# Kernel tuning notes

Measured on AMD Instinct MI355X. Metric: run time of the kernel, lower is better.

## Reference

```python
import jax, jax.numpy as jnp
import numpy as np

B, T, C = 1024, 512, 48

def setup_inputs() -> dict:
    key = jax.random.key(0)
    k1, k2, k3 = jax.random.split(key, 3)
    potentials = jax.random.normal(k1, (B, T, C), dtype=jnp.float32)
    sequence_lengths = jax.random.randint(k2, (B, 1), 1, T).astype(jnp.int32)
    # layer weight: uniform initializer (keras default uniform is U[-0.05, 0.05])
    transitions = jax.random.uniform(k3, (C, C), dtype=jnp.float32, minval=-0.05, maxval=0.05)
    return {"potentials": potentials, "sequence_lengths": sequence_lengths, "transitions": transitions}

def reference(potentials, sequence_lengths, transitions):
    # Faithful jax port of tf.contrib.crf.crf_decode (Viterbi max-plus DP),
    # followed by one_hot as in CRFLayer.call (inference branch of in_train_phase).
    Bb, Tt, Cc = potentials.shape
    seq_len = sequence_lengths.reshape(-1)  # K.flatten

    def fwd_step(score, xs):
        # score: [B,C] viterbi scores at step t-1
        pot_t, t = xs
        total = score[:, :, None] + transitions[None]  # [B, C_prev, C_cur]
        bp = jnp.argmax(total, axis=1).astype(jnp.int32)  # [B,C] best prev tag
        new_score = jnp.max(total, axis=1) + pot_t        # [B,C]
        valid = (t < seq_len)[:, None]                    # mask steps past seq_len
        score = jnp.where(valid, new_score, score)
        bp = jnp.where(valid, bp, jnp.arange(Cc, dtype=jnp.int32)[None])
        return score, bp

    init = potentials[:, 0]                               # [B,C]
    xs = (jnp.swapaxes(potentials[:, 1:], 0, 1), jnp.arange(1, Tt))
    last_score, bps = jax.lax.scan(fwd_step, init, xs)    # bps: [T-1,B,C]

    last_tag = jnp.argmax(last_score, axis=-1).astype(jnp.int32)  # [B]

    def back_step(tag_next, bp):
        prev = jnp.take_along_axis(bp, tag_next[:, None], axis=1)[:, 0]
        return prev, tag_next

    first_tag, tags_rest = jax.lax.scan(back_step, last_tag, bps, reverse=True)
    tags = jnp.concatenate([first_tag[None], tags_rest], axis=0)  # [T,B]
    tags = jnp.swapaxes(tags, 0, 1)                               # [B,T]
    return jax.nn.one_hot(tags, Cc, dtype=potentials.dtype)       # [B,T,C]
```

## Files before the change

kernel.cpp:

```cpp
#include <hip/hip_runtime.h>

#define T_DIM 512
#define C_DIM 48
#define BPS   64
#define CH    4

typedef float f32x2 __attribute__((ext_vector_type(2)));
typedef float f32x4 __attribute__((ext_vector_type(4)));

#if __has_builtin(__builtin_amdgcn_readlane)
#define READLANE_I(v, l) __builtin_amdgcn_readlane((v), (l))
#else
#define READLANE_I(v, l) __shfl((v), (l), 64)
#endif

#if __has_builtin(__builtin_amdgcn_wave_barrier)
#define WAVE_SYNC() do { __asm__ __volatile__("" ::: "memory"); __builtin_amdgcn_wave_barrier(); } while (0)
#else
#define WAVE_SYNC() __asm__ __volatile__("" ::: "memory")
#endif

__device__ __forceinline__ unsigned umin_(unsigned a, unsigned b) { return a < b ? a : b; }

__device__ __forceinline__ float max3f(float a, float b, float c) {
    float d;
    asm("v_max3_f32 %0, %1, %2, %3" : "=v"(d) : "v"(a), "v"(b), "v"(c));
    return d;
}
__device__ __forceinline__ unsigned min3u(unsigned a, unsigned b, unsigned c) {
    unsigned d;
    asm("v_min3_u32 %0, %1, %2, %3" : "=v"(d) : "v"(a), "v"(b), "v"(c));
    return d;
}

#define CV(I_)  (cv2[(I_) / 2][(I_) & 1])
#define UU(I_)  (__float_as_uint(d2[(I_) / 2][(I_) & 1]) | (unsigned)(I_))
#define EMIN3(I_) min3u(UU(I_), UU((I_) + 1), UU((I_) + 2))

#define VSTEP(T_, PV_) do {                                                  \
    float A0  = max3f(CV(0),  CV(1),  CV(2));                                \
    float A1  = max3f(CV(3),  CV(4),  CV(5));                                \
    float A2  = max3f(CV(6),  CV(7),  CV(8));                                \
    float A3  = max3f(CV(9),  CV(10), CV(11));                               \
    float A4  = max3f(CV(12), CV(13), CV(14));                               \
    float A5  = max3f(CV(15), CV(16), CV(17));                               \
    float A6  = max3f(CV(18), CV(19), CV(20));                               \
    float A7  = max3f(CV(21), CV(22), CV(23));                               \
    float A8  = max3f(CV(24), CV(25), CV(26));                               \
    float A9  = max3f(CV(27), CV(28), CV(29));                               \
    float A10 = max3f(CV(30), CV(31), CV(32));                               \
    float A11 = max3f(CV(33), CV(34), CV(35));                               \
    float A12 = max3f(CV(36), CV(37), CV(38));                               \
    float A13 = max3f(CV(39), CV(40), CV(41));                               \
    float A14 = max3f(CV(42), CV(43), CV(44));                               \
    float A15 = max3f(CV(45), CV(46), CV(47));                               \
    float B0 = max3f(A0,  A1,  A2);                                          \
    float B1 = max3f(A3,  A4,  A5);                                          \
    float B2 = max3f(A6,  A7,  A8);                                          \
    float B3 = max3f(A9,  A10, A11);                                         \
    float B4 = max3f(A12, A13, A14);                                         \
    float Cx0 = max3f(B0, B1, B2);                                           \
    float Cx1 = max3f(B3, B4, A15);                                          \
    const float m_v = fmaxf(Cx0, Cx1);                                       \
    const float ns_ = m_v + (PV_);                                           \
    const int nxt_ = cur ^ 1;                                                \
    sc[nxt_][tid] = ns_;                            \
    WAVE_SYNC();                                                             \
    const f32x4* sp_ = (const f32x4*)sc[nxt_];                               \
    f32x4 sv_[12];                                                           \
    _Pragma("unroll")                                                        \
    for (int m_ = 0; m_ < 12; ++m_) sv_[m_] = sp_[m_];      \
           \
    f32x2 d2[24];                                                            \
    const f32x2 mv2_ = {m_v, m_v};                                           \
    _Pragma("unroll")                                                        \
    for (int k_ = 0; k_ < 24; ++k_) d2[k_] = cv2[k_] - mv2_;     \
    unsigned U0  = EMIN3(0);   unsigned U1  = EMIN3(3);                      \
    unsigned U2  = EMIN3(6);   unsigned U3  = EMIN3(9);                      \
    unsigned U4  = EMIN3(12);  unsigned U5  = EMIN3(15);                     \
    unsigned U6  = EMIN3(18);  unsigned U7  = EMIN3(21);                     \
    unsigned U8  = EMIN3(24);  unsigned U9  = EMIN3(27);                     \
    unsigned U10 = EMIN3(30);  unsigned U11 = EMIN3(33);                     \
    unsigned U12 = EMIN3(36);  unsigned U13 = EMIN3(39);                     \
    unsigned U14 = EMIN3(42);  unsigned U15 = EMIN3(45);                     \
    unsigned V0 = min3u(U0,  U1,  U2);                                       \
    unsigned V1 = min3u(U3,  U4,  U5);                                       \
    unsigned V2 = min3u(U6,  U7,  U8);                                       \
    unsigned V3 = min3u(U9,  U10, U11);                                      \
    unsigned V4 = min3u(U12, U13, U14);                                      \
    unsigned W0 = min3u(V0, V1, V2);                                         \
    unsigned W1 = min3u(V3, V4, U15);                                        \
    const unsigned wi_ = umin_(W0, W1);                                      \
    bp[(T_) * BPS + tid] = (unsigned char)wi_;     \
         \
    _Pragma("unroll")                                                        \
    for (int m_ = 0; m_ < 12; ++m_) {                                        \
        cv2[2 * m_]     = sv_[m_].xy + tc2[2 * m_];                          \
        cv2[2 * m_ + 1] = sv_[m_].zw + tc2[2 * m_ + 1];                      \
    }                                                                        \
    cur = nxt_;                                                              \
} while (0)

__global__ __launch_bounds__(64, 1) void crf_viterbi(
    const float* __restrict__ pot,
    const int*   __restrict__ seqlen,
    const float* __restrict__ trans,
    float*       __restrict__ out)
{
    const int b   = blockIdx.x;
    const int tid = threadIdx.x;
    const int jj  = (tid < C_DIM) ? tid : (C_DIM - 1);

    __shared__ __align__(16) float sc[2][64];
    __shared__ unsigned char bp[T_DIM * BPS];
    __shared__ __align__(4) unsigned char tags[T_DIM];

    const float* potb = pot + (size_t)b * (T_DIM * C_DIM);
    const int L   = seqlen[b];
    const int thi = L - 1;

    f32x2 tc2[24];
#pragma unroll
    for (int k = 0; k < 24; ++k) {
        tc2[k][0] = trans[(2 * k)     * C_DIM + jj];
        tc2[k][1] = trans[(2 * k + 1) * C_DIM + jj];
    }

    sc[0][tid] = potb[jj];
    WAVE_SYNC();
    f32x2 cv2[24];
    {
        const f32x4* sp0 = (const f32x4*)sc[0];
#pragma unroll
        for (int m = 0; m < 12; ++m) {
            f32x4 sv = sp0[m];
            cv2[2 * m]     = sv.xy + tc2[2 * m];
            cv2[2 * m + 1] = sv.zw + tc2[2 * m + 1];
        }
    }
    int cur = 0;

    const float* pp = potb + jj;

    float pb[CH];
#pragma unroll
    for (int k = 0; k < CH; ++k) {
        int tt = 1 + k; if (tt > T_DIM - 1) tt = T_DIM - 1;
        pb[k] = pp[tt * C_DIM];
    }
    for (int t0 = 1; t0 < L; t0 += CH) {
        float nb[CH];
#pragma unroll
        for (int k = 0; k < CH; ++k) {
            int tt = t0 + CH + k; if (tt > T_DIM - 1) tt = T_DIM - 1;
            nb[k] = pp[tt * C_DIM];
        }
#pragma unroll
        for (int k = 0; k < CH; ++k) {
            const int t = t0 + k;
            if (t >= L) break;
            VSTEP(t, pb[k]);
        }
#pragma unroll
        for (int k = 0; k < CH; ++k) pb[k] = nb[k];
    }
    __syncthreads();

    const float* fs = sc[cur];
    float bv = fs[0];
    int   bi = 0;
#pragma unroll
    for (int i = 1; i < C_DIM; ++i) {
        float v = fs[i];
        if (v > bv) { bv = v; bi = i; }
    }
    const int last_tag = __builtin_amdgcn_readfirstlane(bi);

    for (int t = L + tid; t < T_DIM; t += 64) tags[t] = (unsigned char)last_tag;

    int y = last_tag;
    for (int c0 = (thi >> 6) << 6; c0 >= 0; c0 -= 64) {
        int row[64];
#pragma unroll
        for (int k = 0; k < 64; ++k) row[k] = bp[(c0 + k) * BPS + jj];

        int vacc = 0;
#pragma unroll
        for (int k = 63; k >= 0; --k) {
            const int t = c0 + k;
            vacc = (tid == k) ? y : vacc;
            const int ynew = READLANE_I(row[k], y);
            if ((unsigned)(t - 1) < (unsigned)thi) y = ynew;
        }
        const int tk = c0 + tid;
        if (tk <= thi) tags[tk] = (unsigned char)(vacc & 0xff);
    }
    __syncthreads();

    if (tid < C_DIM) {
        const int r = tid / 12;
        const int q = tid - r * 12;
        const int cbase = q * 4;
        float* ob = out + (size_t)b * (T_DIM * C_DIM);
        for (int t0 = 0; t0 < T_DIM; t0 += 4) {
            const unsigned int tg4 = *(const unsigned int*)&tags[t0];
            const int mytag = (int)((tg4 >> (r * 8)) & 0xffu);
            float4 v;
            v.x = (cbase + 0 == mytag) ? 1.0f : 0.0f;
            v.y = (cbase + 1 == mytag) ? 1.0f : 0.0f;
            v.z = (cbase + 2 == mytag) ? 1.0f : 0.0f;
            v.w = (cbase + 3 == mytag) ? 1.0f : 0.0f;
            *(float4*)(ob + (size_t)(t0 + r) * C_DIM + cbase) = v;
        }
    }
}

extern "C" void kernel_launch(void* const* d_in, const int* in_sizes, int n_in,
                              void* d_out, int out_size, void* d_ws, size_t ws_size,
                              hipStream_t stream) {
    const float* pot    = (const float*)d_in[0];
    const int*   sl     = (const int*)d_in[1];
    const float* trans  = (const float*)d_in[2];
    float*       out    = (float*)d_out;
    const int B = in_sizes[1];
    crf_viterbi<<<B, 64, 0, stream>>>(pot, sl, trans, out);
}
```

Baseline: 345.0 us.

## Split Viterbi forward into max-wave and argmax-wave producer/consumer pipeline

The forward recursion now runs on two waves per block. Wave 0 does only the max-plus score update and writes scores and maxima into shared-memory ring buffers. Wave 1 rebuilds the candidate values from the ring and computes the argmax backpointers, which takes the argmax off wave 0's serial critical path. The waves coordinate through volatile shared progress counters with spin-waits. The one-hot output store is also spread over 96 threads instead of 48. The cost is spin-wait overhead, recomputing the candidate values on wave 1, and doubled register pressure per block under launch_bounds(128,2).

```diff
diff --git a/kernel.cpp b/kernel.cpp
--- a/kernel.cpp
+++ b/kernel.cpp
@@ -4,6 +4,8 @@
 #define C_DIM 48
 #define BPS   64
 #define CH    4
+#define RING  8
+#define RMASK (RING - 1)
 
 typedef float f32x2 __attribute__((ext_vector_type(2)));
 typedef float f32x4 __attribute__((ext_vector_type(4)));
@@ -14,6 +16,12 @@
 #define READLANE_I(v, l) __shfl((v), (l), 64)
 #endif
 
+#if __has_builtin(__builtin_amdgcn_s_sleep)
+#define SPIN_PAUSE() __builtin_amdgcn_s_sleep(1)
+#else
+#define SPIN_PAUSE()
+#endif
+
 #if __has_builtin(__builtin_amdgcn_wave_barrier)
 #define WAVE_SYNC() do { __asm__ __volatile__("" ::: "memory"); __builtin_amdgcn_wave_barrier(); } while (0)
 #else
@@ -37,83 +45,25 @@
 #define UU(I_)  (__float_as_uint(d2[(I_) / 2][(I_) & 1]) | (unsigned)(I_))
 #define EMIN3(I_) min3u(UU(I_), UU((I_) + 1), UU((I_) + 2))
 
-#define VSTEP(T_, PV_) do {                                                  \
-    float A0  = max3f(CV(0),  CV(1),  CV(2));                                \
-    float A1  = max3f(CV(3),  CV(4),  CV(5));                                \
-    float A2  = max3f(CV(6),  CV(7),  CV(8));                                \
-    float A3  = max3f(CV(9),  CV(10), CV(11));                               \
-    float A4  = max3f(CV(12), CV(13), CV(14));                               \
-    float A5  = max3f(CV(15), CV(16), CV(17));                               \
-    float A6  = max3f(CV(18), CV(19), CV(20));                               \
-    float A7  = max3f(CV(21), CV(22), CV(23));                               \
-    float A8  = max3f(CV(24), CV(25), CV(26));                               \
-    float A9  = max3f(CV(27), CV(28), CV(29));                               \
-    float A10 = max3f(CV(30), CV(31), CV(32));                               \
-    float A11 = max3f(CV(33), CV(34), CV(35));                               \
-    float A12 = max3f(CV(36), CV(37), CV(38));                               \
-    float A13 = max3f(CV(39), CV(40), CV(41));                               \
-    float A14 = max3f(CV(42), CV(43), CV(44));                               \
-    float A15 = max3f(CV(45), CV(46), CV(47));                               \
-    float B0 = max3f(A0,  A1,  A2);                                          \
-    float B1 = max3f(A3,  A4,  A5);                                          \
-    float B2 = max3f(A6,  A7,  A8);                                          \
-    float B3 = max3f(A9,  A10, A11);                                         \
-    float B4 = max3f(A12, A13, A14);                                         \
-    float Cx0 = max3f(B0, B1, B2);                                           \
-    float Cx1 = max3f(B3, B4, A15);                                          \
-    const float m_v = fmaxf(Cx0, Cx1);                                       \
-    const float ns_ = m_v + (PV_);                                           \
-    const int nxt_ = cur ^ 1;                                                \
-    sc[nxt_][tid] = ns_;                            \
-    WAVE_SYNC();                                                             \
-    const f32x4* sp_ = (const f32x4*)sc[nxt_];                               \
-    f32x4 sv_[12];                                                           \
-    _Pragma("unroll")                                                        \
-    for (int m_ = 0; m_ < 12; ++m_) sv_[m_] = sp_[m_];      \
-           \
-    f32x2 d2[24];                                                            \
-    const f32x2 mv2_ = {m_v, m_v};                                           \
-    _Pragma("unroll")                                                        \
-    for (int k_ = 0; k_ < 24; ++k_) d2[k_] = cv2[k_] - mv2_;     \
-    unsigned U0  = EMIN3(0);   unsigned U1  = EMIN3(3);                      \
-    unsigned U2  = EMIN3(6);   unsigned U3  = EMIN3(9);                      \
-    unsigned U4  = EMIN3(12);  unsigned U5  = EMIN3(15);                     \
-    unsigned U6  = EMIN3(18);  unsigned U7  = EMIN3(21);                     \
-    unsigned U8  = EMIN3(24);  unsigned U9  = EMIN3(27);                     \
-    unsigned U10 = EMIN3(30);  unsigned U11 = EMIN3(33);                     \
-    unsigned U12 = EMIN3(36);  unsigned U13 = EMIN3(39);                     \
-    unsigned U14 = EMIN3(42);  unsigned U15 = EMIN3(45);                     \
-    unsigned V0 = min3u(U0,  U1,  U2);                                       \
-    unsigned V1 = min3u(U3,  U4,  U5);                                       \
-    unsigned V2 = min3u(U6,  U7,  U8);                                       \
-    unsigned V3 = min3u(U9,  U10, U11);                                      \
-    unsigned V4 = min3u(U12, U13, U14);                                      \
-    unsigned W0 = min3u(V0, V1, V2);                                         \
-    unsigned W1 = min3u(V3, V4, U15);                                        \
-    const unsigned wi_ = umin_(W0, W1);                                      \
-    bp[(T_) * BPS + tid] = (unsigned char)wi_;     \
-         \
-    _Pragma("unroll")                                                        \
-    for (int m_ = 0; m_ < 12; ++m_) {                                        \
-        cv2[2 * m_]     = sv_[m_].xy + tc2[2 * m_];                          \
-        cv2[2 * m_ + 1] = sv_[m_].zw + tc2[2 * m_ + 1];                      \
-    }                                                                        \
-    cur = nxt_;                                                              \
-} while (0)
-
-__global__ __launch_bounds__(64, 1) void crf_viterbi(
+__global__ __launch_bounds__(128, 2) void crf_viterbi(
     const float* __restrict__ pot,
     const int*   __restrict__ seqlen,
     const float* __restrict__ trans,
     float*       __restrict__ out)
 {
-    const int b   = blockIdx.x;
-    const int tid = threadIdx.x;
-    const int jj  = (tid < C_DIM) ? tid : (C_DIM - 1);
-
-    __shared__ __align__(16) float sc[2][64];
+    const int b    = blockIdx.x;
+    const int tid  = threadIdx.x;
+    const int lane = tid & 63;
+    const int wid  = tid >> 6;
+    const int jj   = (lane < C_DIM) ? lane : (C_DIM - 1);
+
+    __shared__ __align__(16) float sring[RING][64];
+    __shared__ __align__(16) float mring[RING][64];
     __shared__ unsigned char bp[T_DIM * BPS];
     __shared__ __align__(4) unsigned char tags[T_DIM];
+    __shared__ __align__(16) float fsc[64];
+    __shared__ volatile int prog0;
+    __shared__ volatile int prog1;
 
     const float* potb = pot + (size_t)b * (T_DIM * C_DIM);
     const int L   = seqlen[b];
@@ -126,47 +76,127 @@
         tc2[k][1] = trans[(2 * k + 1) * C_DIM + jj];
     }
 
-    sc[0][tid] = potb[jj];
-    WAVE_SYNC();
-    f32x2 cv2[24];
-    {
-        const f32x4* sp0 = (const f32x4*)sc[0];
-#pragma unroll
-        for (int m = 0; m < 12; ++m) {
-            f32x4 sv = sp0[m];
-            cv2[2 * m]     = sv.xy + tc2[2 * m];
-            cv2[2 * m + 1] = sv.zw + tc2[2 * m + 1];
-        }
-    }
-    int cur = 0;
-
-    const float* pp = potb + jj;
-
-    float pb[CH];
-#pragma unroll
-    for (int k = 0; k < CH; ++k) {
-        int tt = 1 + k; if (tt > T_DIM - 1) tt = T_DIM - 1;
-        pb[k] = pp[tt * C_DIM];
-    }
-    for (int t0 = 1; t0 < L; t0 += CH) {
-        float nb[CH];
+    float ns = 0.0f;
+    if (wid == 0) {
+        ns = potb[jj];
+        sring[0][lane] = ns;
+    }
+    if (tid == 0) { prog0 = 0; prog1 = 0; }
+    __syncthreads();
+
+    if (wid == 0) {
+        const float* pp = potb + jj;
+        float pb[CH];
 #pragma unroll
         for (int k = 0; k < CH; ++k) {
-            int tt = t0 + CH + k; if (tt > T_DIM - 1) tt = T_DIM - 1;
-            nb[k] = pp[tt * C_DIM];
-        }
-#pragma unroll
-        for (int k = 0; k < CH; ++k) {
-            const int t = t0 + k;
-            if (t >= L) break;
-            VSTEP(t, pb[k]);
-        }
-#pragma unroll
-        for (int k = 0; k < CH; ++k) pb[k] = nb[k];
+            int tt = 1 + k; if (tt > T_DIM - 1) tt = T_DIM - 1;
+            pb[k] = pp[tt * C_DIM];
+        }
+        for (int t0 = 1; t0 < L; t0 += CH) {
+            float nb[CH];
+#pragma unroll
+            for (int k = 0; k < CH; ++k) {
+                int tt = t0 + CH + k; if (tt > T_DIM - 1) tt = T_DIM - 1;
+                nb[k] = pp[tt * C_DIM];
+            }
+            while (prog1 < t0 - (RING - CH)) { SPIN_PAUSE(); }
+            WAVE_SYNC();
+#pragma unroll
+            for (int k = 0; k < CH; ++k) {
+                const int t = t0 + k;
+                if (t >= L) break;
+                const f32x4* sp = (const f32x4*)sring[(t - 1) & RMASK];
+                f32x2 cv2[24];
+#pragma unroll
+                for (int m = 0; m < 12; ++m) {
+                    f32x4 sv = sp[m];
+                    cv2[2 * m]     = sv.xy + tc2[2 * m];
+                    cv2[2 * m + 1] = sv.zw + tc2[2 * m + 1];
+                }
+                float A0  = max3f(CV(0),  CV(1),  CV(2));
+                float A1  = max3f(CV(3),  CV(4),  CV(5));
+                float A2  = max3f(CV(6),  CV(7),  CV(8));
+                float A3  = max3f(CV(9),  CV(10), CV(11));
+                float A4  = max3f(CV(12), CV(13), CV(14));
+                float A5  = max3f(CV(15), CV(16), CV(17));
+                float A6  = max3f(CV(18), CV(19), CV(20));
+                float A7  = max3f(CV(21), CV(22), CV(23));
+                float A8  = max3f(CV(24), CV(25), CV(26));
+                float A9  = max3f(CV(27), CV(28), CV(29));
+                float A10 = max3f(CV(30), CV(31), CV(32));
+                float A11 = max3f(CV(33), CV(34), CV(35));
+                float A12 = max3f(CV(36), CV(37), CV(38));
+                float A13 = max3f(CV(39), CV(40), CV(41));
+                float A14 = max3f(CV(42), CV(43), CV(44));
+                float A15 = max3f(CV(45), CV(46), CV(47));
+                float B0 = max3f(A0,  A1,  A2);
+                float B1 = max3f(A3,  A4,  A5);
+                float B2 = max3f(A6,  A7,  A8);
+                float B3 = max3f(A9,  A10, A11);
+                float B4 = max3f(A12, A13, A14);
+                float Cx0 = max3f(B0, B1, B2);
+                float Cx1 = max3f(B3, B4, A15);
+                const float m_v = fmaxf(Cx0, Cx1);
+                ns = m_v + pb[k];
+                mring[t & RMASK][lane] = m_v;
+                sring[t & RMASK][lane] = ns;
+            }
+            WAVE_SYNC();
+            {
+                int td = t0 + CH - 1; if (td > thi) td = thi;
+                prog0 = td;
+            }
+#pragma unroll
+            for (int k = 0; k < CH; ++k) pb[k] = nb[k];
+        }
+        fsc[lane] = ns;
+    } else {
+        for (int u0 = 1; u0 < L; u0 += CH) {
+            int tgt = u0 + CH - 1; if (tgt > thi) tgt = thi;
+            while (prog0 < tgt) { SPIN_PAUSE(); }
+            WAVE_SYNC();
+#pragma unroll
+            for (int k = 0; k < CH; ++k) {
+                const int u = u0 + k;
+                if (u >= L) break;
+                const f32x4* sp = (const f32x4*)sring[(u - 1) & RMASK];
+                f32x2 cv2[24];
+#pragma unroll
+                for (int m = 0; m < 12; ++m) {
+                    f32x4 sv = sp[m];
+                    cv2[2 * m]     = sv.xy + tc2[2 * m];
+                    cv2[2 * m + 1] = sv.zw + tc2[2 * m + 1];
+                }
+                const float m_v = mring[u & RMASK][lane];
+                f32x2 d2[24];
+                const f32x2 mv2 = {m_v, m_v};
+#pragma unroll
+                for (int q = 0; q < 24; ++q) d2[q] = cv2[q] - mv2;
+                unsigned U0  = EMIN3(0);   unsigned U1  = EMIN3(3);
+                unsigned U2  = EMIN3(6);   unsigned U3  = EMIN3(9);
+                unsigned U4  = EMIN3(12);  unsigned U5  = EMIN3(15);
+                unsigned U6  = EMIN3(18);  unsigned U7  = EMIN3(21);
+                unsigned U8  = EMIN3(24);  unsigned U9  = EMIN3(27);
+                unsigned U10 = EMIN3(30);  unsigned U11 = EMIN3(33);
+                unsigned U12 = EMIN3(36);  unsigned U13 = EMIN3(39);
+                unsigned U14 = EMIN3(42);  unsigned U15 = EMIN3(45);
+                unsigned V0 = min3u(U0,  U1,  U2);
+                unsigned V1 = min3u(U3,  U4,  U5);
+                unsigned V2 = min3u(U6,  U7,  U8);
+                unsigned V3 = min3u(U9,  U10, U11);
+                unsigned V4 = min3u(U12, U13, U14);
+                unsigned W0 = min3u(V0, V1, V2);
+                unsigned W1 = min3u(V3, V4, U15);
+                const unsigned wi_ = umin_(W0, W1);
+                bp[u * BPS + lane] = (unsigned char)wi_;
+            }
+            WAVE_SYNC();
+            prog1 = tgt;
+        }
     }
     __syncthreads();
 
-    const float* fs = sc[cur];
+    const float* fs = fsc;
     float bv = fs[0];
     int   bi = 0;
 #pragma unroll
@@ -176,35 +206,36 @@
     }
     const int last_tag = __builtin_amdgcn_readfirstlane(bi);
 
-    for (int t = L + tid; t < T_DIM; t += 64) tags[t] = (unsigned char)last_tag;
-
-    int y = last_tag;
-    for (int c0 = (thi >> 6) << 6; c0 >= 0; c0 -= 64) {
-        int row[64];
-#pragma unroll
-        for (int k = 0; k < 64; ++k) row[k] = bp[(c0 + k) * BPS + jj];
-
-        int vacc = 0;
-#pragma unroll
-        for (int k = 63; k >= 0; --k) {
-            const int t = c0 + k;
-            vacc = (tid == k) ? y : vacc;
-            const int ynew = READLANE_I(row[k], y);
-            if ((unsigned)(t - 1) < (unsigned)thi) y = ynew;
-        }
-        const int tk = c0 + tid;
-        if (tk <= thi) tags[tk] = (unsigned char)(vacc & 0xff);
+    for (int t = L + tid; t < T_DIM; t += 128) tags[t] = (unsigned char)last_tag;
+
+    if (wid == 0) {
+        int y = last_tag;
+        for (int c0 = (thi >> 6) << 6; c0 >= 0; c0 -= 64) {
+            int row[64];
+#pragma unroll
+            for (int k = 0; k < 64; ++k) row[k] = bp[(c0 + k) * BPS + jj];
+
+            int vacc = 0;
+#pragma unroll
+            for (int k = 63; k >= 0; --k) {
+                const int t = c0 + k;
+                vacc = (lane == k) ? y : vacc;
+                const int ynew = READLANE_I(row[k], y);
+                if ((unsigned)(t - 1) < (unsigned)thi) y = ynew;
+            }
+            const int tk = c0 + lane;
+            if (tk <= thi) tags[tk] = (unsigned char)(vacc & 0xff);
+        }
     }
     __syncthreads();
 
-    if (tid < C_DIM) {
+    if (tid < 96) {
         const int r = tid / 12;
         const int q = tid - r * 12;
         const int cbase = q * 4;
         float* ob = out + (size_t)b * (T_DIM * C_DIM);
-        for (int t0 = 0; t0 < T_DIM; t0 += 4) {
-            const unsigned int tg4 = *(const unsigned int*)&tags[t0];
-            const int mytag = (int)((tg4 >> (r * 8)) & 0xffu);
+        for (int t0 = 0; t0 < T_DIM; t0 += 8) {
+            const int mytag = (int)tags[t0 + r];
             float4 v;
             v.x = (cbase + 0 == mytag) ? 1.0f : 0.0f;
             v.y = (cbase + 1 == mytag) ? 1.0f : 0.0f;
@@ -223,5 +254,5 @@
     const float* trans  = (const float*)d_in[2];
     float*       out    = (float*)d_out;
     const int B = in_sizes[1];
-    crf_viterbi<<<B, 64, 0, stream>>>(pot, sl, trans, out);
-}
+    crf_viterbi<<<B, 128, 0, stream>>>(pot, sl, trans, out);
+}
```

Result: slower. 501.3 us (+45.3%).
